# Performance work log

Hardware: AMD Instinct MI355X
Metric: run time of the kernel (lower is better)

Reference implementation:

```python
import jax, jax.numpy as jnp
import numpy as np

B, S, HID = 2, 1024, 4096
NH, NKV, HD = 32, 8, 128
EPS = 1e-6
ROPE_THETA = 1000000.0
SCALE = HD ** -0.5
NREP = NH // NKV


def _rope_tables(batch, seq, head_dim, theta):
    inv_freq = 1.0 / (theta ** (np.arange(0, head_dim, 2, dtype=np.float32) / head_dim))
    pos = np.arange(seq, dtype=np.float32)
    freqs = np.outer(pos, inv_freq)            # [S, HD/2]
    emb = np.concatenate([freqs, freqs], -1)   # [S, HD]
    cos = np.broadcast_to(np.cos(emb), (batch, seq, head_dim))
    sin = np.broadcast_to(np.sin(emb), (batch, seq, head_dim))
    return jnp.asarray(cos), jnp.asarray(sin)


def setup_inputs() -> dict:
    key = jax.random.key(0)
    k1, k2, k3 = jax.random.split(key, 3)
    hidden_states = jax.random.normal(k1, (B, S, HID), dtype=jnp.float32)
    cos, sin = _rope_tables(B, S, HD, ROPE_THETA)
    attention_mask = jnp.ones((B, 1, S, S), dtype=bool)
    w_qkv = jax.random.normal(k2, ((NH + 2 * NKV) * HD, HID), dtype=jnp.float32) * (HID ** -0.5)
    w_q_norm = jnp.ones((HD,), dtype=jnp.float32)
    w_k_norm = jnp.ones((HD,), dtype=jnp.float32)
    w_o = jax.random.normal(k3, (HID, NH * HD), dtype=jnp.float32) * ((NH * HD) ** -0.5)
    return {"hidden_states": hidden_states, "cos": cos, "sin": sin,
            "attention_mask": attention_mask, "w_qkv": w_qkv,
            "w_q_norm": w_q_norm, "w_k_norm": w_k_norm, "w_o": w_o}


def _rms_norm(x, w):
    var = jnp.mean(jnp.square(x), axis=-1, keepdims=True)
    return x * jax.lax.rsqrt(var + EPS) * w


def _rotate_half(x):
    x1, x2 = jnp.split(x, 2, axis=-1)
    return jnp.concatenate([-x2, x1], axis=-1)


def reference(hidden_states, cos, sin, attention_mask, w_qkv, w_q_norm, w_k_norm, w_o):
    qkv = jnp.einsum('bsh,oh->bso', hidden_states, w_qkv)  # [B,S,(NH+2NKV)*HD]
    q, k, v = jnp.split(qkv, [NH * HD, (NH + NKV) * HD], axis=-1)
    q = _rms_norm(q.reshape(B, S, NH, HD), w_q_norm).transpose(0, 2, 1, 3)   # [B,NH,S,HD]
    k = _rms_norm(k.reshape(B, S, NKV, HD), w_k_norm).transpose(0, 2, 1, 3)  # [B,NKV,S,HD]
    v = v.reshape(B, S, NKV, HD).transpose(0, 2, 1, 3)                        # [B,NKV,S,HD]
    c = cos[:, None, :, :]
    s = sin[:, None, :, :]
    q = q * c + _rotate_half(q) * s
    k = k * c + _rotate_half(k) * s
    k = jnp.repeat(k, NREP, axis=1)  # GQA repeat -> [B,NH,S,HD]
    v = jnp.repeat(v, NREP, axis=1)
    scores = jnp.einsum('bhqd,bhkd->bhqk', q, k) * SCALE
    scores = jnp.where(attention_mask, scores, jnp.finfo(scores.dtype).min)
    attn = jax.nn.softmax(scores, axis=-1)
    out = jnp.einsum('bhqk,bhkd->bhqd', attn, v)
    out = out.transpose(0, 2, 1, 3).reshape(B, S, NH * HD)
    return jnp.einsum('bsd,od->bso', out, w_o)
```

## Files before the change

kernel.cpp:

```cpp
#include <hip/hip_runtime.h>
#include <hip/hip_bf16.h>

typedef __bf16 bf16_t;
typedef bf16_t bf16x2 __attribute__((ext_vector_type(2)));
typedef bf16_t bf16x8 __attribute__((ext_vector_type(8)));
typedef float f32x4 __attribute__((ext_vector_type(4)));

#define DEVI __device__ __forceinline__

DEVI void gld_lds16(const void* g, void* l) {
  __builtin_amdgcn_global_load_lds(
      (const __attribute__((address_space(1))) void*)g,
      (__attribute__((address_space(3))) void*)l, 16, 0, 0);
}

__global__ __launch_bounds__(256) void cvt_f32_bf16(
    const float* __restrict__ in, bf16_t* __restrict__ out, long n) {
  long i = ((long)blockIdx.x * 256 + threadIdx.x) * 8;
  if (i >= n) return;
  float4 a = *(const float4*)(in + i);
  float4 b = *(const float4*)(in + i + 4);
  bf16x8 v = {(__bf16)a.x, (__bf16)a.y, (__bf16)a.z, (__bf16)a.w,
              (__bf16)b.x, (__bf16)b.y, (__bf16)b.z, (__bf16)b.w};
  *(bf16x8*)(out + i) = v;
}

template <int FC, int MINW, typename CT>
__global__ __launch_bounds__(512, MINW) void gemm128(
    const bf16_t* __restrict__ A, const bf16_t* __restrict__ W,
    CT* __restrict__ C, int M, int N, int K) {
  constexpr int BN = FC * 64;
  constexpr int P1 = FC / 2, P2 = FC - P1;
  __shared__ __align__(16) bf16_t As[2][128 * 64];
  __shared__ __align__(16) bf16_t Bs[2][BN * 64];
  const int tid = threadIdx.x, wave = tid >> 6, lane = tid & 63;
  const int q16 = lane & 15, gq = lane >> 4, sw = q16 & 7;
  const int wm = wave >> 2, wn = wave & 3;
  const int nM = M >> 7, nN = N / BN;
  const int cM = nM >> 1, cN = nN >> 2;
  const int xcd = (int)blockIdx.x & 7, wi = (int)blockIdx.x >> 3;
  const int tm = ((xcd >> 2) * cM + wi / cN) << 7;
  const int tn = ((xcd & 3) * cN + wi % cN) * BN;
  const int NT = K >> 6;
  const bf16_t* Ag = A + (size_t)tm * K;
  const bf16_t* Wg = W + (size_t)tn * K;
  const int sr = (wave << 3) + (lane >> 3);
  const int scol = (((lane & 7) ^ (sr & 7)) << 3);

#define STG(gbase, kq, uu, ldsbuf)                              \
  gld_lds16((gbase) + (size_t)((uu)*64 + sr) * K + (kq) + scol, \
            &(ldsbuf)[0] + (uu)*4096 + (wave << 9))

  f32x4 acc[4][FC];
#pragma unroll
  for (int i = 0; i < 4; ++i)
#pragma unroll
    for (int j = 0; j < FC; ++j) acc[i][j] = f32x4{0.f, 0.f, 0.f, 0.f};

  STG(Ag, 0, 0, As[0]);
  STG(Ag, 0, 1, As[0]);
#pragma unroll
  for (int u = 0; u < FC; ++u) STG(Wg, 0, u, Bs[0]);
  STG(Ag, 64, 0, As[1]);
  STG(Ag, 64, 1, As[1]);
  asm volatile("s_waitcnt vmcnt(2)" ::: "memory");
  __builtin_amdgcn_s_barrier();

  for (int t = 0; t < NT; ++t) {
    const int cur = t & 1;
    const bf16_t* Acur = As[cur];
    const bf16_t* Bcur = Bs[cur];
    const int k1 = (t + 1) << 6, k2 = (t + 2) << 6;
    bf16x8 afr[4][2];

#pragma unroll
    for (int fr = 0; fr < 4; ++fr) {
      const bf16_t* rp = Acur + (wm * 64 + fr * 16 + q16) * 64;
      afr[fr][0] = *(const bf16x8*)(rp + ((gq ^ sw) << 3));
      afr[fr][1] = *(const bf16x8*)(rp + (((4 + gq) ^ sw) << 3));
    }
    bf16x8 b1[P1][2];
#pragma unroll
    for (int fc = 0; fc < P1; ++fc) {
      const bf16_t* rp = Bcur + (wn * (16 * FC) + fc * 16 + q16) * 64;
      b1[fc][0] = *(const bf16x8*)(rp + ((gq ^ sw) << 3));
      b1[fc][1] = *(const bf16x8*)(rp + (((4 + gq) ^ sw) << 3));
    }
    if (t + 1 < NT) {
#pragma unroll
      for (int u = 0; u < FC; ++u) STG(Wg, k1, u, Bs[cur ^ 1]);
    }
    __builtin_amdgcn_s_barrier();
    __builtin_amdgcn_s_setprio(1);
#pragma unroll
    for (int fr = 0; fr < 4; ++fr)
#pragma unroll
      for (int fc = 0; fc < P1; ++fc)
#pragma unroll
        for (int kk = 0; kk < 2; ++kk)
          acc[fr][fc] = __builtin_amdgcn_mfma_f32_16x16x32_bf16(
              afr[fr][kk], b1[fc][kk], acc[fr][fc], 0, 0, 0);
    __builtin_amdgcn_s_setprio(0);
    asm volatile("" ::: "memory");
    __builtin_amdgcn_s_barrier();

    bf16x8 b2[P2][2];
#pragma unroll
    for (int f2 = 0; f2 < P2; ++f2) {
      const bf16_t* rp = Bcur + (wn * (16 * FC) + (P1 + f2) * 16 + q16) * 64;
      b2[f2][0] = *(const bf16x8*)(rp + ((gq ^ sw) << 3));
      b2[f2][1] = *(const bf16x8*)(rp + (((4 + gq) ^ sw) << 3));
    }
    if (t + 2 < NT) {
      STG(Ag, k2, 0, As[cur]);
      STG(Ag, k2, 1, As[cur]);
    }
    __builtin_amdgcn_s_barrier();
    __builtin_amdgcn_s_setprio(1);
#pragma unroll
    for (int fr = 0; fr < 4; ++fr)
#pragma unroll
      for (int f2 = 0; f2 < P2; ++f2)
#pragma unroll
        for (int kk = 0; kk < 2; ++kk)
          acc[fr][P1 + f2] = __builtin_amdgcn_mfma_f32_16x16x32_bf16(
              afr[fr][kk], b2[f2][kk], acc[fr][P1 + f2], 0, 0, 0);
    __builtin_amdgcn_s_setprio(0);
    if (t + 2 < NT)
      asm volatile("s_waitcnt vmcnt(2)" ::: "memory");
    else
      asm volatile("s_waitcnt vmcnt(0)" ::: "memory");
    __builtin_amdgcn_s_barrier();
  }

#pragma unroll
  for (int fr = 0; fr < 4; ++fr)
#pragma unroll
    for (int fc = 0; fc < FC; ++fc)
#pragma unroll
      for (int i = 0; i < 4; ++i) {
        int row = tm + wm * 64 + fr * 16 + gq * 4 + i;
        int col = tn + wn * (16 * FC) + fc * 16 + q16;
        C[(size_t)row * N + col] = (CT)acc[fr][fc][i];
      }
#undef STG
}

__global__ __launch_bounds__(256) void rope_scatter(
    const bf16_t* __restrict__ qkv, const float* __restrict__ cosb,
    const float* __restrict__ sinb, const float* __restrict__ wq,
    const float* __restrict__ wk, bf16_t* __restrict__ qb,
    bf16_t* __restrict__ kb, bf16_t* __restrict__ vt) {
  const int row = blockIdx.x;
  const int b = row >> 10, s = row & 1023;
  const int wave = threadIdx.x >> 6, lane = threadIdx.x & 63;
  const int d0 = 2 * lane;
  const float c0 = cosb[(size_t)row * 128 + d0];
  const float c1 = cosb[(size_t)row * 128 + d0 + 1];
  const float s0 = sinb[(size_t)row * 128 + d0];
  const float s1 = sinb[(size_t)row * 128 + d0 + 1];
  const float g0q = wq[d0], g1q = wq[d0 + 1];
  const float g0k = wk[d0], g1k = wk[d0 + 1];
  const float sign = (lane < 32) ? -1.f : 1.f;

  for (int h = wave; h < 32; h += 4) {
    const bf16_t* x = qkv + (size_t)row * 6144 + h * 128 + d0;
    float x0 = (float)x[0], x1 = (float)x[1];
    float ss = x0 * x0 + x1 * x1;
#pragma unroll
    for (int off = 1; off < 64; off <<= 1) ss += __shfl_xor(ss, off);
    float r = rsqrtf(ss * (1.0f / 128.0f) + 1e-6f);
    float n0 = x0 * r * g0q, n1 = x1 * r * g1q;
    float o0 = __shfl_xor(n0, 32), o1 = __shfl_xor(n1, 32);
    float y0 = n0 * c0 + sign * o0 * s0;
    float y1 = n1 * c1 + sign * o1 * s1;
    bf16_t* dst = qb + ((size_t)(b * 32 + h) * 1024 + s) * 128 + d0;
    dst[0] = (__bf16)y0;
    dst[1] = (__bf16)y1;
  }
  for (int h = wave; h < 8; h += 4) {
    const bf16_t* x = qkv + (size_t)row * 6144 + 4096 + h * 128 + d0;
    float x0 = (float)x[0], x1 = (float)x[1];
    float ss = x0 * x0 + x1 * x1;
#pragma unroll
    for (int off = 1; off < 64; off <<= 1) ss += __shfl_xor(ss, off);
    float r = rsqrtf(ss * (1.0f / 128.0f) + 1e-6f);
    float n0 = x0 * r * g0k, n1 = x1 * r * g1k;
    float o0 = __shfl_xor(n0, 32), o1 = __shfl_xor(n1, 32);
    float y0 = n0 * c0 + sign * o0 * s0;
    float y1 = n1 * c1 + sign * o1 * s1;
    bf16_t* dst = kb + ((size_t)(b * 8 + h) * 1024 + s) * 128 + d0;
    dst[0] = (__bf16)y0;
    dst[1] = (__bf16)y1;
  }
  for (int h = wave; h < 8; h += 4) {
    const bf16_t* x = qkv + (size_t)row * 6144 + 5120 + h * 128 + d0;
    bf16_t* dst = vt + ((size_t)(b * 8 + h) * 128 + d0) * 1024 + s;
    dst[0] = x[0];
    dst[1024] = x[1];
  }
}

__global__ __launch_bounds__(256, 2) void attn_fwd(
    const bf16_t* __restrict__ Qb, const bf16_t* __restrict__ Kb,
    const bf16_t* __restrict__ Vt, bf16_t* __restrict__ Ob) {
  __shared__ __align__(16) bf16_t Kl[2][64 * 128];
  __shared__ __align__(16) bf16_t Vl[2][128 * 64];
  __shared__ __align__(16) bf16_t Pl[4][32 * 64];
  const int tid = threadIdx.x, wave = tid >> 6, lane = tid & 63;
  const int q16 = lane & 15, g = lane >> 4;
  const int bid = blockIdx.x;
  const int bh = bid >> 3, qt = bid & 7;
  const int b = bh >> 5, h = bh & 31;
  const int kvh = (b << 3) + (h >> 2);
  const bf16_t* qp = Qb + ((size_t)bh * 1024 + qt * 128 + wave * 32) * 128;
  const bf16_t* kp = Kb + (size_t)kvh * (1024 * 128);
  const bf16_t* vp = Vt + (size_t)kvh * (128 * 1024);
  const float SCALE = 0.088388347648318447f;
  const int sw = q16 & 7;

  bf16x8 qf[2][4];
#pragma unroll
  for (int m = 0; m < 2; ++m)
#pragma unroll
    for (int kc = 0; kc < 4; ++kc)
      qf[m][kc] = *(const bf16x8*)(qp + (m * 16 + q16) * 128 + kc * 32 + g * 8);

  f32x4 oacc[2][8];
#pragma unroll
  for (int m = 0; m < 2; ++m)
#pragma unroll
    for (int dc = 0; dc < 8; ++dc) oacc[m][dc] = f32x4{0.f, 0.f, 0.f, 0.f};
  float m_run[2] = {-3.0e38f, -3.0e38f}, l_run[2] = {0.f, 0.f};

#define STAGE_KV(buf, jj)                                                      \
  {                                                                            \
    _Pragma("unroll") for (int i = 0; i < 4; ++i) {                            \
      int n = (wave * 4 + i) * 64 + lane;                                      \
      int rk = n >> 4, ck = (n & 15) ^ (rk & 7);                               \
      gld_lds16(kp + (size_t)((jj) + rk) * 128 + ck * 8,                       \
                &Kl[buf][0] + (wave * 4 + i) * 512);                           \
      int rv = n >> 3, cv = (n & 7) ^ (rv & 7);                                \
      gld_lds16(vp + (size_t)rv * 1024 + (jj) + cv * 8,                        \
                &Vl[buf][0] + (wave * 4 + i) * 512);                           \
    }                                                                          \
  }

  STAGE_KV(0, 0);
  __syncthreads();
  int cur = 0;

  for (int jt = 0; jt < 16; ++jt) {
    if (jt < 15) STAGE_KV(cur ^ 1, (jt + 1) * 64);

    const bf16_t* Kc = &Kl[cur][0];
    const bf16_t* Vc = &Vl[cur][0];
    bf16_t* Plw = &Pl[wave][0];

    f32x4 st[2][4];
#pragma unroll
    for (int m = 0; m < 2; ++m)
#pragma unroll
      for (int t = 0; t < 4; ++t) st[m][t] = f32x4{0.f, 0.f, 0.f, 0.f};
#pragma unroll
    for (int t = 0; t < 4; ++t) {
      bf16x8 kf[4];
#pragma unroll
      for (int kc = 0; kc < 4; ++kc)
        kf[kc] = *(const bf16x8*)(Kc + (t * 16 + q16) * 128 + (((kc * 4 + g) ^ sw) << 3));
#pragma unroll
      for (int m = 0; m < 2; ++m)
#pragma unroll
        for (int kc = 0; kc < 4; ++kc)
          st[m][t] = __builtin_amdgcn_mfma_f32_16x16x32_bf16(kf[kc], qf[m][kc], st[m][t], 0, 0, 0);
    }

#pragma unroll
    for (int m = 0; m < 2; ++m) {
      float mx = m_run[m];
#pragma unroll
      for (int t = 0; t < 4; ++t)
#pragma unroll
        for (int i = 0; i < 4; ++i) {
          float s = st[m][t][i] * SCALE;
          st[m][t][i] = s;
          mx = fmaxf(mx, s);
        }
      mx = fmaxf(mx, __shfl_xor(mx, 16));
      mx = fmaxf(mx, __shfl_xor(mx, 32));
      float alpha = __expf(m_run[m] - mx);
      float lsum = 0.f;
      const int prow = m * 16 + q16;
#pragma unroll
      for (int t = 0; t < 4; ++t) {
        float p0 = __expf(st[m][t][0] - mx);
        float p1 = __expf(st[m][t][1] - mx);
        float p2 = __expf(st[m][t][2] - mx);
        float p3 = __expf(st[m][t][3] - mx);
        lsum += (p0 + p1) + (p2 + p3);
        int k0 = t * 16 + g * 4;
        int a0 = prow * 64 + ((((k0 >> 3)) ^ sw) << 3) + (k0 & 7);
        *(bf16x2*)(Plw + a0) = bf16x2{(__bf16)p0, (__bf16)p1};
        *(bf16x2*)(Plw + a0 + 2) = bf16x2{(__bf16)p2, (__bf16)p3};
      }
      lsum += __shfl_xor(lsum, 16);
      lsum += __shfl_xor(lsum, 32);
      l_run[m] = l_run[m] * alpha + lsum;
      m_run[m] = mx;
      float ar[4];
#pragma unroll
      for (int i = 0; i < 4; ++i) ar[i] = __shfl(alpha, g * 4 + i);
#pragma unroll
      for (int dc = 0; dc < 8; ++dc)
#pragma unroll
        for (int i = 0; i < 4; ++i) oacc[m][dc][i] *= ar[i];
    }

#pragma unroll
    for (int ks = 0; ks < 2; ++ks) {
      bf16x8 pf0 = *(const bf16x8*)(Plw + (q16)*64 + (((ks * 4 + g) ^ sw) << 3));
      bf16x8 pf1 = *(const bf16x8*)(Plw + (16 + q16) * 64 + (((ks * 4 + g) ^ sw) << 3));
#pragma unroll
      for (int dc = 0; dc < 8; ++dc) {
        bf16x8 vf = *(const bf16x8*)(Vc + (dc * 16 + q16) * 64 + (((ks * 4 + g) ^ sw) << 3));
        oacc[0][dc] = __builtin_amdgcn_mfma_f32_16x16x32_bf16(pf0, vf, oacc[0][dc], 0, 0, 0);
        oacc[1][dc] = __builtin_amdgcn_mfma_f32_16x16x32_bf16(pf1, vf, oacc[1][dc], 0, 0, 0);
      }
    }

    __syncthreads();
    cur ^= 1;
  }

  const int rowbase = (b << 10) + qt * 128 + wave * 32;
#pragma unroll
  for (int m = 0; m < 2; ++m) {
    float lr[4];
#pragma unroll
    for (int i = 0; i < 4; ++i) lr[i] = __shfl(l_run[m], g * 4 + i);
#pragma unroll
    for (int dc = 0; dc < 8; ++dc)
#pragma unroll
      for (int i = 0; i < 4; ++i) {
        int row = rowbase + m * 16 + g * 4 + i;
        int col = (h << 7) + dc * 16 + q16;
        Ob[(size_t)row * 4096 + col] = (__bf16)(oacc[m][dc][i] / lr[i]);
      }
  }
#undef STAGE_KV
}

extern "C" void kernel_launch(void* const* d_in, const int* in_sizes, int n_in,
                              void* d_out, int out_size, void* d_ws,
                              size_t ws_size, hipStream_t stream) {
  const float* hidden = (const float*)d_in[0];
  const float* cosb = (const float*)d_in[1];
  const float* sinb = (const float*)d_in[2];
  const float* w_qkv = (const float*)d_in[4];
  const float* w_qn = (const float*)d_in[5];
  const float* w_kn = (const float*)d_in[6];
  const float* w_o = (const float*)d_in[7];
  float* out = (float*)d_out;

  char* ws = (char*)d_ws;
  bf16_t* wqkvb = (bf16_t*)ws;
  bf16_t* wob = (bf16_t*)ws;
  bf16_t* qb = (bf16_t*)(ws + 33554432);
  bf16_t* hb = (bf16_t*)(ws + 50331648);
  bf16_t* attno = hb;
  bf16_t* qkv = (bf16_t*)(ws + 67108864);
  bf16_t* kb = (bf16_t*)(ws + 92274688);
  bf16_t* vt = (bf16_t*)(ws + 96468992);

  cvt_f32_bf16<<<dim3(8388608 / 8 / 256), dim3(256), 0, stream>>>(hidden, hb, 8388608);
  cvt_f32_bf16<<<dim3(25165824 / 8 / 256), dim3(256), 0, stream>>>(w_qkv, wqkvb, 25165824);
  gemm128<3, 4, bf16_t><<<dim3(512), dim3(512), 0, stream>>>(hb, wqkvb, qkv, 2048, 6144, 4096);
  cvt_f32_bf16<<<dim3(16777216 / 8 / 256), dim3(256), 0, stream>>>(w_o, wob, 16777216);
  rope_scatter<<<dim3(2048), dim3(256), 0, stream>>>(qkv, cosb, sinb, w_qn, w_kn, qb, kb, vt);
  attn_fwd<<<dim3(64 * 8), dim3(256), 0, stream>>>(qb, kb, vt, attno);
  gemm128<2, 4, float><<<dim3(512), dim3(512), 0, stream>>>(attno, wob, out, 2048, 4096, 4096);
}
```

Baseline: 284.4 us.

## Fuse fp32-to-bf16 conversion into GEMM loads, dropping separate convert kernels

Removes the three standalone fp32-to-bf16 conversion kernels for hidden states, w_qkv and w_o. The GEMMs now read fp32 operands from global memory into registers, convert them to bf16 and write them to LDS, so the extra round trip through bf16 workspace is gone. This replaces async global-to-LDS loads with register-staged loads and changes the barrier and wait pattern inside the main loop. The trade-offs are higher register pressure, twice the global read bytes per tile for the fp32 operands, and reconverting each weight tile for every M-tile that reads it.

```diff
diff --git a/kernel.cpp b/kernel.cpp
--- a/kernel.cpp
+++ b/kernel.cpp
@@ -14,23 +14,17 @@
       (__attribute__((address_space(3))) void*)l, 16, 0, 0);
 }
 
-__global__ __launch_bounds__(256) void cvt_f32_bf16(
-    const float* __restrict__ in, bf16_t* __restrict__ out, long n) {
-  long i = ((long)blockIdx.x * 256 + threadIdx.x) * 8;
-  if (i >= n) return;
-  float4 a = *(const float4*)(in + i);
-  float4 b = *(const float4*)(in + i + 4);
-  bf16x8 v = {(__bf16)a.x, (__bf16)a.y, (__bf16)a.z, (__bf16)a.w,
-              (__bf16)b.x, (__bf16)b.y, (__bf16)b.z, (__bf16)b.w};
-  *(bf16x8*)(out + i) = v;
-}
-
-template <int FC, int MINW, typename CT>
-__global__ __launch_bounds__(512, MINW) void gemm128(
-    const bf16_t* __restrict__ A, const bf16_t* __restrict__ W,
+DEVI bf16x8 cvt8(f32x4 a, f32x4 b) {
+  return bf16x8{(__bf16)a[0], (__bf16)a[1], (__bf16)a[2], (__bf16)a[3],
+                (__bf16)b[0], (__bf16)b[1], (__bf16)b[2], (__bf16)b[3]};
+}
+
+template <int FC, bool AF32, typename CT>
+__global__ __launch_bounds__(512, 4) void gemmf(
+    const void* __restrict__ Av, const float* __restrict__ Wf,
     CT* __restrict__ C, int M, int N, int K) {
   constexpr int BN = FC * 64;
-  constexpr int P1 = FC / 2, P2 = FC - P1;
+  constexpr int P1 = 1, P2 = FC - 1;
   __shared__ __align__(16) bf16_t As[2][128 * 64];
   __shared__ __align__(16) bf16_t Bs[2][BN * 64];
   const int tid = threadIdx.x, wave = tid >> 6, lane = tid & 63;
@@ -42,14 +36,38 @@
   const int tm = ((xcd >> 2) * cM + wi / cN) << 7;
   const int tn = ((xcd & 3) * cN + wi % cN) * BN;
   const int NT = K >> 6;
-  const bf16_t* Ag = A + (size_t)tm * K;
-  const bf16_t* Wg = W + (size_t)tn * K;
+  const float* Agf = (const float*)Av + (size_t)tm * K;
+  const bf16_t* Agb = (const bf16_t*)Av + (size_t)tm * K;
+  const float* Wg = Wf + (size_t)tn * K;
   const int sr = (wave << 3) + (lane >> 3);
-  const int scol = (((lane & 7) ^ (sr & 7)) << 3);
-
-#define STG(gbase, kq, uu, ldsbuf)                              \
-  gld_lds16((gbase) + (size_t)((uu)*64 + sr) * K + (kq) + scol, \
-            &(ldsbuf)[0] + (uu)*4096 + (wave << 9))
+  const int c8 = (lane & 7) * 8;
+  const int swz8 = (((lane & 7) ^ (sr & 7)) << 3);
+  const int ldsoff = sr * 64 + swz8;
+
+#define AISSUE(kq, rg)                                              \
+  {                                                                 \
+    _Pragma("unroll") for (int u = 0; u < 2; ++u) {                 \
+      const float* p = Agf + (size_t)(u * 64 + sr) * K + (kq) + c8; \
+      rg[u][0] = *(const f32x4*)p;                                  \
+      rg[u][1] = *(const f32x4*)(p + 4);                            \
+    }                                                               \
+  }
+#define BISSUE(kq, rg)                                             \
+  {                                                                \
+    _Pragma("unroll") for (int u = 0; u < FC; ++u) {               \
+      const float* p = Wg + (size_t)(u * 64 + sr) * K + (kq) + c8; \
+      rg[u][0] = *(const f32x4*)p;                                 \
+      rg[u][1] = *(const f32x4*)(p + 4);                           \
+    }                                                              \
+  }
+#define WRU(base, u, rg) \
+  *(bf16x8*)(&(base)[0] + (u)*4096 + ldsoff) = cvt8(rg[u][0], rg[u][1]);
+#define AGLD(kq, buf)                                            \
+  {                                                              \
+    _Pragma("unroll") for (int u = 0; u < 2; ++u)                \
+        gld_lds16(Agb + (size_t)(u * 64 + sr) * K + (kq) + swz8, \
+                  &As[buf][0] + u * 4096 + (wave << 9));         \
+  }
 
   f32x4 acc[4][FC];
 #pragma unroll
@@ -57,13 +75,28 @@
 #pragma unroll
     for (int j = 0; j < FC; ++j) acc[i][j] = f32x4{0.f, 0.f, 0.f, 0.f};
 
-  STG(Ag, 0, 0, As[0]);
-  STG(Ag, 0, 1, As[0]);
-#pragma unroll
-  for (int u = 0; u < FC; ++u) STG(Wg, 0, u, Bs[0]);
-  STG(Ag, 64, 0, As[1]);
-  STG(Ag, 64, 1, As[1]);
-  asm volatile("s_waitcnt vmcnt(2)" ::: "memory");
+  f32x4 arg[2][2], brg[FC][2];
+
+  if constexpr (AF32) {
+    f32x4 a1g[2][2];
+    AISSUE(0, arg);
+    BISSUE(0, brg);
+    AISSUE(64, a1g);
+    WRU(As[0], 0, arg);
+    WRU(As[0], 1, arg);
+#pragma unroll
+    for (int u = 0; u < FC; ++u) WRU(Bs[0], u, brg);
+    WRU(As[1], 0, a1g);
+    WRU(As[1], 1, a1g);
+  } else {
+    AGLD(0, 0);
+    AGLD(64, 1);
+    BISSUE(0, brg);
+    asm volatile("s_waitcnt vmcnt(0)" ::: "memory");
+#pragma unroll
+    for (int u = 0; u < FC; ++u) WRU(Bs[0], u, brg);
+  }
+  asm volatile("s_waitcnt lgkmcnt(0)" ::: "memory");
   __builtin_amdgcn_s_barrier();
 
   for (int t = 0; t < NT; ++t) {
@@ -73,6 +106,11 @@
     const int k1 = (t + 1) << 6, k2 = (t + 2) << 6;
     bf16x8 afr[4][2];
 
+    if constexpr (AF32) {
+      if (t + 2 < NT) AISSUE(k2, arg);
+    }
+    if (t + 1 < NT) BISSUE(k1, brg);
+    __builtin_amdgcn_sched_barrier(0);
 #pragma unroll
     for (int fr = 0; fr < 4; ++fr) {
       const bf16_t* rp = Acur + (wm * 64 + fr * 16 + q16) * 64;
@@ -86,11 +124,8 @@
       b1[fc][0] = *(const bf16x8*)(rp + ((gq ^ sw) << 3));
       b1[fc][1] = *(const bf16x8*)(rp + (((4 + gq) ^ sw) << 3));
     }
-    if (t + 1 < NT) {
-#pragma unroll
-      for (int u = 0; u < FC; ++u) STG(Wg, k1, u, Bs[cur ^ 1]);
-    }
     __builtin_amdgcn_s_barrier();
+
     __builtin_amdgcn_s_setprio(1);
 #pragma unroll
     for (int fr = 0; fr < 4; ++fr)
@@ -101,8 +136,20 @@
           acc[fr][fc] = __builtin_amdgcn_mfma_f32_16x16x32_bf16(
               afr[fr][kk], b1[fc][kk], acc[fr][fc], 0, 0, 0);
     __builtin_amdgcn_s_setprio(0);
-    asm volatile("" ::: "memory");
-    __builtin_amdgcn_s_barrier();
+    __builtin_amdgcn_sched_barrier(0);
+    asm volatile("s_waitcnt vmcnt(0)" ::: "memory");
+    if (t + 1 < NT) {
+#pragma unroll
+      for (int u = 0; u < FC; ++u) WRU(Bs[cur ^ 1], u, brg);
+    }
+    if constexpr (AF32) {
+      if (t + 2 < NT) {
+        WRU(As[cur], 0, arg);
+        WRU(As[cur], 1, arg);
+      }
+    } else {
+      if (t + 2 < NT) AGLD(k2, cur);
+    }
 
     bf16x8 b2[P2][2];
 #pragma unroll
@@ -111,11 +158,6 @@
       b2[f2][0] = *(const bf16x8*)(rp + ((gq ^ sw) << 3));
       b2[f2][1] = *(const bf16x8*)(rp + (((4 + gq) ^ sw) << 3));
     }
-    if (t + 2 < NT) {
-      STG(Ag, k2, 0, As[cur]);
-      STG(Ag, k2, 1, As[cur]);
-    }
-    __builtin_amdgcn_s_barrier();
     __builtin_amdgcn_s_setprio(1);
 #pragma unroll
     for (int fr = 0; fr < 4; ++fr)
@@ -126,10 +168,7 @@
           acc[fr][P1 + f2] = __builtin_amdgcn_mfma_f32_16x16x32_bf16(
               afr[fr][kk], b2[f2][kk], acc[fr][P1 + f2], 0, 0, 0);
     __builtin_amdgcn_s_setprio(0);
-    if (t + 2 < NT)
-      asm volatile("s_waitcnt vmcnt(2)" ::: "memory");
-    else
-      asm volatile("s_waitcnt vmcnt(0)" ::: "memory");
+    asm volatile("s_waitcnt lgkmcnt(0)" ::: "memory");
     __builtin_amdgcn_s_barrier();
   }
 
@@ -143,7 +182,10 @@
         int col = tn + wn * (16 * FC) + fc * 16 + q16;
         C[(size_t)row * N + col] = (CT)acc[fr][fc][i];
       }
-#undef STG
+#undef AISSUE
+#undef BISSUE
+#undef WRU
+#undef AGLD
 }
 
 __global__ __launch_bounds__(256) void rope_scatter(
@@ -363,20 +405,16 @@
   float* out = (float*)d_out;
 
   char* ws = (char*)d_ws;
-  bf16_t* wqkvb = (bf16_t*)ws;
-  bf16_t* wob = (bf16_t*)ws;
-  bf16_t* qb = (bf16_t*)(ws + 33554432);
-  bf16_t* hb = (bf16_t*)(ws + 50331648);
-  bf16_t* attno = hb;
-  bf16_t* qkv = (bf16_t*)(ws + 67108864);
-  bf16_t* kb = (bf16_t*)(ws + 92274688);
-  bf16_t* vt = (bf16_t*)(ws + 96468992);
-
-  cvt_f32_bf16<<<dim3(8388608 / 8 / 256), dim3(256), 0, stream>>>(hidden, hb, 8388608);
-  cvt_f32_bf16<<<dim3(25165824 / 8 / 256), dim3(256), 0, stream>>>(w_qkv, wqkvb, 25165824);
-  gemm128<3, 4, bf16_t><<<dim3(512), dim3(512), 0, stream>>>(hb, wqkvb, qkv, 2048, 6144, 4096);
-  cvt_f32_bf16<<<dim3(16777216 / 8 / 256), dim3(256), 0, stream>>>(w_o, wob, 16777216);
+  bf16_t* qkv = (bf16_t*)ws;
+  bf16_t* qb = (bf16_t*)(ws + 25165824);
+  bf16_t* kb = (bf16_t*)(ws + 41943040);
+  bf16_t* vt = (bf16_t*)(ws + 46137344);
+  bf16_t* attno = (bf16_t*)(ws + 50331648);
+
+  gemmf<3, true, bf16_t><<<dim3(512), dim3(512), 0, stream>>>(
+      hidden, w_qkv, qkv, 2048, 6144, 4096);
   rope_scatter<<<dim3(2048), dim3(256), 0, stream>>>(qkv, cosb, sinb, w_qn, w_kn, qb, kb, vt);
   attn_fwd<<<dim3(64 * 8), dim3(256), 0, stream>>>(qb, kb, vt, attno);
-  gemm128<2, 4, float><<<dim3(512), dim3(512), 0, stream>>>(attno, wob, out, 2048, 4096, 4096);
-}
+  gemmf<2, false, float><<<dim3(512), dim3(512), 0, stream>>>(
+      attno, w_o, out, 2048, 4096, 4096);
+}
```

Result: slower. 832.0 us (+192.6%).
